# Kernel tuning notes

Measured on AMD Instinct MI355X. Metric: run time of the kernel, lower is better.

Reference implementation:

```python
import jax, jax.numpy as jnp
import numpy as np

N = 200_000   # total nodes across batch
D = 256       # input_dim (feature size)
B = 1024      # batch_size (number of graphs)
N_ITERS = 6


def setup_inputs() -> dict:
    key = jax.random.key(0)
    k0, k1, k2, k3, k4, k5 = jax.random.split(key, 6)
    s = 1.0 / np.sqrt(D)  # pytorch LSTM init: U(-1/sqrt(hidden), 1/sqrt(hidden))
    feat = jax.random.normal(k0, (N, D), dtype=jnp.float32)
    segment_ids = jnp.sort(jax.random.randint(k1, (N,), 0, B, dtype=jnp.int32))
    W_ih = jax.random.uniform(k2, (4 * D, 2 * D), minval=-s, maxval=s, dtype=jnp.float32)
    W_hh = jax.random.uniform(k3, (4 * D, D), minval=-s, maxval=s, dtype=jnp.float32)
    b_ih = jax.random.uniform(k4, (4 * D,), minval=-s, maxval=s, dtype=jnp.float32)
    b_hh = jax.random.uniform(k5, (4 * D,), minval=-s, maxval=s, dtype=jnp.float32)
    return {"feat": feat, "W_ih": W_ih, "W_hh": W_hh, "b_ih": b_ih,
            "b_hh": b_hh, "segment_ids": segment_ids, "batch_size": B}


def reference(feat, W_ih, W_hh, b_ih, b_hh, segment_ids, batch_size):
    H = W_hh.shape[1]
    dt = feat.dtype
    h = jnp.zeros((batch_size, H), dtype=dt)
    c = jnp.zeros((batch_size, H), dtype=dt)
    q_star = jnp.zeros((batch_size, 2 * H), dtype=dt)
    for _ in range(N_ITERS):
        # single-layer LSTM step on a length-1 sequence (pytorch gate order i,f,g,o)
        gates = q_star @ W_ih.T + h @ W_hh.T + b_ih + b_hh  # [B, 4H]
        gi, gf, gg, go = jnp.split(gates, 4, axis=-1)
        c = jax.nn.sigmoid(gf) * c + jax.nn.sigmoid(gi) * jnp.tanh(gg)
        h = jax.nn.sigmoid(go) * jnp.tanh(c)
        q = h  # [B, H]
        # e_i = <x_i, q_{graph(i)}>  (broadcast_nodes + dot)
        e = jnp.sum(feat * q[segment_ids], axis=-1)  # [N]
        # segment-wise stable softmax (softmax_nodes)
        emax = jax.ops.segment_max(e, segment_ids, num_segments=batch_size)
        ex = jnp.exp(e - emax[segment_ids])
        denom = jax.ops.segment_sum(ex, segment_ids, num_segments=batch_size)
        alpha = ex / denom[segment_ids]  # [N]
        # weighted sum readout (sum_nodes)
        readout = jax.ops.segment_sum(feat * alpha[:, None], segment_ids,
                                      num_segments=batch_size)  # [B, H]
        q_star = jnp.concatenate([q, readout], axis=-1)  # [B, 2H]
    return q_star
```

## Files before the change

kernel.cpp:

```cpp
#include <hip/hip_runtime.h>
#include <hip/hip_bf16.h>
#include <hip/hip_fp16.h>
#include <stdint.h>

#define D    256
#define K2   512
#define G4   1024

typedef __attribute__((ext_vector_type(8))) short  short8;
typedef __attribute__((ext_vector_type(4))) float  float4v;

__device__ inline short f2bf(float v) {
    __hip_bfloat16 b = __float2bfloat16(v);
    union { __hip_bfloat16 b; unsigned short u; } cv; cv.b = b;
    return (short)cv.u;
}
__device__ inline float bfs2f(short s) {
    union { unsigned int i; float f; } v;
    v.i = ((unsigned int)(unsigned short)s) << 16;
    return v.f;
}

__device__ inline float wave_sum64(float x) {
    union { float f; int i; } c, t;
#define DPP_ADD(CTRL, RM)                                                     \
    c.f = x;                                                                  \
    t.i = __builtin_amdgcn_update_dpp(0, c.i, (CTRL), (RM), 0xf, true);       \
    x += t.f;
    DPP_ADD(0x111, 0xf)
    DPP_ADD(0x112, 0xf)
    DPP_ADD(0x114, 0xf)
    DPP_ADD(0x118, 0xf)
    DPP_ADD(0x142, 0xa)
    DPP_ADD(0x143, 0xc)
#undef DPP_ADD
    union { float f; int i; } r; r.f = x;
    r.i = __builtin_amdgcn_readlane(r.i, 63);
    return r.f;
}

__global__ void k_bounds(const int* __restrict__ seg, int N, int B,
                         int* __restrict__ start) {
    int g = blockIdx.x * blockDim.x + threadIdx.x;
    if (g > B) return;
    int lo = 0, hi = N;
    while (lo < hi) { int mid = (lo + hi) >> 1; if (seg[mid] < g) lo = mid + 1; else hi = mid; }
    start[g] = lo;
}

__global__ void k_cvt(const float* __restrict__ feat, __half* __restrict__ feat16,
                      int total) {
    int i = (blockIdx.x * blockDim.x + threadIdx.x) * 8;
    int stride = gridDim.x * blockDim.x * 8;
    for (; i < total; i += stride) {
        float4v a = *(const float4v*)(feat + i);
        float4v b = *(const float4v*)(feat + i + 4);
        union { __half2 h2[4]; uint4 u; } o;
        o.h2[0] = __floats2half2_rn(a.x, a.y);
        o.h2[1] = __floats2half2_rn(a.z, a.w);
        o.h2[2] = __floats2half2_rn(b.x, b.y);
        o.h2[3] = __floats2half2_rn(b.z, b.w);
        *(uint4*)(feat16 + i) = o.u;
    }
}

__global__ void k_prep(const float* __restrict__ Wih,
                       const float* __restrict__ Whh,
                       const float* __restrict__ bih,
                       const float* __restrict__ bhh,
                       short* __restrict__ Wch, short* __restrict__ Wcl,
                       float* __restrict__ bsum) {
    int idx = blockIdx.x * blockDim.x + threadIdx.x;
    if (idx >= G4 * K2) return;
    int r = idx >> 9, cc = idx & (K2 - 1);
    float v = Wih[idx];
    if (cc < D) v += Whh[r * D + cc];
    short hi = f2bf(v);
    Wch[idx] = hi;
    Wcl[idx] = f2bf(v - bfs2f(hi));
    if (idx < G4) bsum[idx] = bih[idx] + bhh[idx];
}

__global__ __launch_bounds__(256) void k_gemm_lstm(
        const short* __restrict__ Xh, const short* __restrict__ Xl,
        const short* __restrict__ Wch, const short* __restrict__ Wcl,
        const float* __restrict__ bsum,
        float* __restrict__ c, float* __restrict__ h) {
    int wave = threadIdx.x >> 6, lane = threadIdx.x & 63;
    int row = lane & 15, quad = lane >> 4;
    int m0 = blockIdx.x * 16;
    int jbase = blockIdx.y * 64 + wave * 16;
    const short* pah = Xh  + (size_t)(m0 + row) * K2 + quad * 8;
    const short* pal = Xl  + (size_t)(m0 + row) * K2 + quad * 8;
    const short* pbh = Wch + (size_t)(jbase + row) * K2 + quad * 8;
    const short* pbl = Wcl + (size_t)(jbase + row) * K2 + quad * 8;
    float4v acc0 = {0,0,0,0}, acc1 = {0,0,0,0}, acc2 = {0,0,0,0}, acc3 = {0,0,0,0};
#pragma unroll
    for (int k = 0; k < K2; k += 32) {
        short8 ahi = *(const short8*)(pah + k);
        short8 alo = *(const short8*)(pal + k);
#define GATE_MFMA(ACC, OFF)                                                        \
        {                                                                          \
            short8 bh = *(const short8*)(pbh + (size_t)(OFF) * K2 + k);            \
            short8 bl = *(const short8*)(pbl + (size_t)(OFF) * K2 + k);            \
            ACC = __builtin_amdgcn_mfma_f32_16x16x32_bf16(ahi, bh, ACC, 0, 0, 0);  \
            ACC = __builtin_amdgcn_mfma_f32_16x16x32_bf16(alo, bh, ACC, 0, 0, 0);  \
            ACC = __builtin_amdgcn_mfma_f32_16x16x32_bf16(ahi, bl, ACC, 0, 0, 0);  \
        }
        GATE_MFMA(acc0, 0)
        GATE_MFMA(acc1, 256)
        GATE_MFMA(acc2, 512)
        GATE_MFMA(acc3, 768)
#undef GATE_MFMA
    }
    int j = jbase + (lane & 15);
    float bi = bsum[j], bf_ = bsum[j + 256], bg = bsum[j + 512], bo = bsum[j + 768];
#pragma unroll
    for (int i = 0; i < 4; i++) {
        int m = m0 + quad * 4 + i;
        size_t ix = (size_t)m * D + j;
        float gi = acc0[i] + bi, gf = acc1[i] + bf_, gg = acc2[i] + bg, go = acc3[i] + bo;
        float si = 1.f / (1.f + __expf(-gi));
        float sf = 1.f / (1.f + __expf(-gf));
        float so = 1.f / (1.f + __expf(-go));
        float cn = sf * c[ix] + si * tanhf(gg);
        float hn = so * tanhf(cn);
        c[ix] = cn;
        h[ix] = hn;
    }
}

__global__ __launch_bounds__(256) void k_attn(const __half* __restrict__ feat16,
                                              const int* __restrict__ start,
                                              const float* __restrict__ h,
                                              float* __restrict__ X,
                                              short* __restrict__ Xh,
                                              short* __restrict__ Xl, int N) {
    __shared__ float accs[4 * D];
    __shared__ float ms[4], ls[4];
    int g = blockIdx.x;
    int t = threadIdx.x;
    int lane = t & 63, wave = t >> 6;
    float hv = h[(size_t)g * D + t];
    {
        size_t ox = (size_t)g * K2 + t;
        X[ox] = hv;
        short hi = f2bf(hv);
        Xh[ox] = hi;
        Xl[ox] = f2bf(hv - bfs2f(hi));
    }
    int s = start[g], e = start[g + 1];
    s = max(0, min(s, N)); e = max(s, min(e, N));
    int cnt = e - s;
    if (cnt <= 0) {
        size_t ox = (size_t)g * K2 + D + t;
        X[ox] = 0.f; Xh[ox] = 0; Xl[ox] = 0;
        return;
    }
    const float NEG = -3.0e38f;
    float4v q = *(const float4v*)(h + (size_t)g * D + lane * 4);
    float m = NEG, l = 0.f;
    float4v acc = {0.f, 0.f, 0.f, 0.f};

    for (int n0 = wave * 4; n0 < cnt; n0 += 16) {
        uint2 raw[4];
#pragma unroll
        for (int r = 0; r < 4; r++) {
            int idx = n0 + r;
            int ci = (idx < cnt) ? (s + idx) : s;
            raw[r] = *((const uint2*)(feat16 + (size_t)ci * D) + lane);
        }
        float4v rows[4];
        float ev[4];
#pragma unroll
        for (int r = 0; r < 4; r++) {
            union { uint2 u; __half2 h2[2]; } cv; cv.u = raw[r];
            float2 f01 = __half22float2(cv.h2[0]);
            float2 f23 = __half22float2(cv.h2[1]);
            rows[r].x = f01.x; rows[r].y = f01.y; rows[r].z = f23.x; rows[r].w = f23.y;
            ev[r] = rows[r].x * q.x + rows[r].y * q.y + rows[r].z * q.z + rows[r].w * q.w;
        }
#pragma unroll
        for (int r = 0; r < 4; r++) ev[r] = wave_sum64(ev[r]);
        float mnew = m;
#pragma unroll
        for (int r = 0; r < 4; r++) {
            if (n0 + r >= cnt) ev[r] = NEG;
            mnew = fmaxf(mnew, ev[r]);
        }
        float alpha = __expf(m - mnew);
        float w[4];
        float wsum = 0.f;
#pragma unroll
        for (int r = 0; r < 4; r++) {
            w[r] = (n0 + r < cnt) ? __expf(ev[r] - mnew) : 0.f;
            wsum += w[r];
        }
        l = l * alpha + wsum;
        acc.x *= alpha; acc.y *= alpha; acc.z *= alpha; acc.w *= alpha;
#pragma unroll
        for (int r = 0; r < 4; r++) {
            acc.x += w[r] * rows[r].x;
            acc.y += w[r] * rows[r].y;
            acc.z += w[r] * rows[r].z;
            acc.w += w[r] * rows[r].w;
        }
        m = mnew;
    }

    *((float4v*)(accs + wave * D + lane * 4)) = acc;
    if (lane == 0) { ms[wave] = m; ls[wave] = l; }
    __syncthreads();
    float mt = fmaxf(fmaxf(ms[0], ms[1]), fmaxf(ms[2], ms[3]));
    float s0 = __expf(ms[0] - mt), s1 = __expf(ms[1] - mt);
    float s2 = __expf(ms[2] - mt), s3 = __expf(ms[3] - mt);
    float lt = ls[0] * s0 + ls[1] * s1 + ls[2] * s2 + ls[3] * s3;
    float val = (accs[t] * s0 + accs[D + t] * s1
               + accs[2 * D + t] * s2 + accs[3 * D + t] * s3) / lt;
    size_t ox = (size_t)g * K2 + D + t;
    X[ox] = val;
    short hi = f2bf(val);
    Xh[ox] = hi;
    Xl[ox] = f2bf(val - bfs2f(hi));
}

extern "C" void kernel_launch(void* const* d_in, const int* in_sizes, int n_in,
                              void* d_out, int out_size, void* d_ws, size_t ws_size,
                              hipStream_t stream) {
    const float* feat = (const float*)d_in[0];
    const float* Wih  = (const float*)d_in[1];
    const float* Whh  = (const float*)d_in[2];
    const float* bih  = (const float*)d_in[3];
    const float* bhh  = (const float*)d_in[4];
    const int*   seg  = (const int*)d_in[5];
    const int N = in_sizes[5];
    const int B = out_size / K2;
    const int total = N * D;

    char* ws = (char*)d_ws;
    size_t szC = (size_t)B * D * sizeof(float);
    float* c   = (float*)ws;
    float* h   = (float*)(ws + szC);
    short* Xh  = (short*)(ws + 2 * szC);
    short* Xl  = (short*)(ws + 2 * szC + (size_t)B * K2 * sizeof(short));
    short* Wch = (short*)(ws + 2 * szC + 2 * (size_t)B * K2 * sizeof(short));
    short* Wcl = (short*)((char*)Wch + (size_t)G4 * K2 * sizeof(short));
    float* bsum = (float*)((char*)Wcl + (size_t)G4 * K2 * sizeof(short));
    int*   start = (int*)((char*)bsum + (size_t)G4 * sizeof(float));
    __half* feat16 = (__half*)(ws + (size_t)16 * 1024 * 1024);

    float* X = (float*)d_out;

    hipMemsetAsync(ws, 0, 2 * szC + 2 * (size_t)B * K2 * sizeof(short), stream);
    k_cvt<<<8192, 256, 0, stream>>>(feat, feat16, total);
    k_prep<<<(G4 * K2 + 255) / 256, 256, 0, stream>>>(Wih, Whh, bih, bhh, Wch, Wcl, bsum);
    k_bounds<<<(B + 1 + 255) / 256, 256, 0, stream>>>(seg, N, B, start);

    for (int it = 0; it < 6; it++) {
        k_gemm_lstm<<<dim3(B / 16, 4), 256, 0, stream>>>(Xh, Xl, Wch, Wcl, bsum, c, h);
        k_attn<<<B, 256, 0, stream>>>(feat16, start, h, X, Xh, Xl, N);
    }
}
```

Baseline: 566.7 us.

## Fuse fp16 feature conversion into first attention pass; split LSTM GEMM across more blocks

```diff
diff --git a/kernel.cpp b/kernel.cpp
--- a/kernel.cpp
+++ b/kernel.cpp
@@ -48,22 +48,6 @@
     start[g] = lo;
 }
 
-__global__ void k_cvt(const float* __restrict__ feat, __half* __restrict__ feat16,
-                      int total) {
-    int i = (blockIdx.x * blockDim.x + threadIdx.x) * 8;
-    int stride = gridDim.x * blockDim.x * 8;
-    for (; i < total; i += stride) {
-        float4v a = *(const float4v*)(feat + i);
-        float4v b = *(const float4v*)(feat + i + 4);
-        union { __half2 h2[4]; uint4 u; } o;
-        o.h2[0] = __floats2half2_rn(a.x, a.y);
-        o.h2[1] = __floats2half2_rn(a.z, a.w);
-        o.h2[2] = __floats2half2_rn(b.x, b.y);
-        o.h2[3] = __floats2half2_rn(b.z, b.w);
-        *(uint4*)(feat16 + i) = o.u;
-    }
-}
-
 __global__ void k_prep(const float* __restrict__ Wih,
                        const float* __restrict__ Whh,
                        const float* __restrict__ bih,
@@ -81,7 +65,7 @@
     if (idx < G4) bsum[idx] = bih[idx] + bhh[idx];
 }
 
-__global__ __launch_bounds__(256) void k_gemm_lstm(
+__global__ __launch_bounds__(256, 4) void k_gemm_lstm(
         const short* __restrict__ Xh, const short* __restrict__ Xl,
         const short* __restrict__ Wch, const short* __restrict__ Wcl,
         const float* __restrict__ bsum,
@@ -89,53 +73,52 @@
     int wave = threadIdx.x >> 6, lane = threadIdx.x & 63;
     int row = lane & 15, quad = lane >> 4;
     int m0 = blockIdx.x * 16;
-    int jbase = blockIdx.y * 64 + wave * 16;
+    int jb = blockIdx.y * 16;
+    int wrow = wave * 256 + jb + row;
     const short* pah = Xh  + (size_t)(m0 + row) * K2 + quad * 8;
     const short* pal = Xl  + (size_t)(m0 + row) * K2 + quad * 8;
-    const short* pbh = Wch + (size_t)(jbase + row) * K2 + quad * 8;
-    const short* pbl = Wcl + (size_t)(jbase + row) * K2 + quad * 8;
-    float4v acc0 = {0,0,0,0}, acc1 = {0,0,0,0}, acc2 = {0,0,0,0}, acc3 = {0,0,0,0};
+    const short* pbh = Wch + (size_t)wrow * K2 + quad * 8;
+    const short* pbl = Wcl + (size_t)wrow * K2 + quad * 8;
+    float4v acc = {0, 0, 0, 0};
 #pragma unroll
     for (int k = 0; k < K2; k += 32) {
         short8 ahi = *(const short8*)(pah + k);
         short8 alo = *(const short8*)(pal + k);
-#define GATE_MFMA(ACC, OFF)                                                        \
-        {                                                                          \
-            short8 bh = *(const short8*)(pbh + (size_t)(OFF) * K2 + k);            \
-            short8 bl = *(const short8*)(pbl + (size_t)(OFF) * K2 + k);            \
-            ACC = __builtin_amdgcn_mfma_f32_16x16x32_bf16(ahi, bh, ACC, 0, 0, 0);  \
-            ACC = __builtin_amdgcn_mfma_f32_16x16x32_bf16(alo, bh, ACC, 0, 0, 0);  \
-            ACC = __builtin_amdgcn_mfma_f32_16x16x32_bf16(ahi, bl, ACC, 0, 0, 0);  \
-        }
-        GATE_MFMA(acc0, 0)
-        GATE_MFMA(acc1, 256)
-        GATE_MFMA(acc2, 512)
-        GATE_MFMA(acc3, 768)
-#undef GATE_MFMA
-    }
-    int j = jbase + (lane & 15);
-    float bi = bsum[j], bf_ = bsum[j + 256], bg = bsum[j + 512], bo = bsum[j + 768];
-#pragma unroll
-    for (int i = 0; i < 4; i++) {
-        int m = m0 + quad * 4 + i;
-        size_t ix = (size_t)m * D + j;
-        float gi = acc0[i] + bi, gf = acc1[i] + bf_, gg = acc2[i] + bg, go = acc3[i] + bo;
-        float si = 1.f / (1.f + __expf(-gi));
-        float sf = 1.f / (1.f + __expf(-gf));
-        float so = 1.f / (1.f + __expf(-go));
-        float cn = sf * c[ix] + si * tanhf(gg);
-        float hn = so * tanhf(cn);
-        c[ix] = cn;
-        h[ix] = hn;
-    }
-}
-
-__global__ __launch_bounds__(256) void k_attn(const __half* __restrict__ feat16,
-                                              const int* __restrict__ start,
-                                              const float* __restrict__ h,
-                                              float* __restrict__ X,
-                                              short* __restrict__ Xh,
-                                              short* __restrict__ Xl, int N) {
+        short8 bh  = *(const short8*)(pbh + k);
+        short8 bl  = *(const short8*)(pbl + k);
+        acc = __builtin_amdgcn_mfma_f32_16x16x32_bf16(ahi, bh, acc, 0, 0, 0);
+        acc = __builtin_amdgcn_mfma_f32_16x16x32_bf16(alo, bh, acc, 0, 0, 0);
+        acc = __builtin_amdgcn_mfma_f32_16x16x32_bf16(ahi, bl, acc, 0, 0, 0);
+    }
+    __shared__ float gl[4][16][17];
+#pragma unroll
+    for (int i = 0; i < 4; i++) gl[wave][quad * 4 + i][row] = acc[i];
+    __syncthreads();
+    int t = threadIdx.x;
+    int mi = t >> 4, jj = t & 15;
+    int j = jb + jj;
+    float gi = gl[0][mi][jj] + bsum[j];
+    float gf = gl[1][mi][jj] + bsum[j + 256];
+    float gg = gl[2][mi][jj] + bsum[j + 512];
+    float go = gl[3][mi][jj] + bsum[j + 768];
+    size_t ix = (size_t)(m0 + mi) * D + j;
+    float si = 1.f / (1.f + __expf(-gi));
+    float sf = 1.f / (1.f + __expf(-gf));
+    float so = 1.f / (1.f + __expf(-go));
+    float cn = sf * c[ix] + si * tanhf(gg);
+    float hn = so * tanhf(cn);
+    c[ix] = cn;
+    h[ix] = hn;
+}
+
+template <bool FIRST>
+__global__ __launch_bounds__(256) void k_attn_t(const float* __restrict__ feat32,
+                                                __half* __restrict__ feat16,
+                                                const int* __restrict__ start,
+                                                const float* __restrict__ h,
+                                                float* __restrict__ X,
+                                                short* __restrict__ Xh,
+                                                short* __restrict__ Xl, int N) {
     __shared__ float accs[4 * D];
     __shared__ float ms[4], ls[4];
     int g = blockIdx.x;
@@ -163,23 +146,44 @@
     float4v acc = {0.f, 0.f, 0.f, 0.f};
 
     for (int n0 = wave * 4; n0 < cnt; n0 += 16) {
-        uint2 raw[4];
-#pragma unroll
-        for (int r = 0; r < 4; r++) {
-            int idx = n0 + r;
-            int ci = (idx < cnt) ? (s + idx) : s;
-            raw[r] = *((const uint2*)(feat16 + (size_t)ci * D) + lane);
-        }
         float4v rows[4];
+        if (FIRST) {
+#pragma unroll
+            for (int r = 0; r < 4; r++) {
+                int idx = n0 + r;
+                int ci = (idx < cnt) ? (s + idx) : s;
+                rows[r] = *((const float4v*)(feat32 + (size_t)ci * D) + lane);
+            }
+#pragma unroll
+            for (int r = 0; r < 4; r++) {
+                int idx = n0 + r;
+                if (idx < cnt) {
+                    union { uint2 u; __half2 h2[2]; } cv;
+                    cv.h2[0] = __floats2half2_rn(rows[r].x, rows[r].y);
+                    cv.h2[1] = __floats2half2_rn(rows[r].z, rows[r].w);
+                    *((uint2*)(feat16 + (size_t)(s + idx) * D) + lane) = cv.u;
+                }
+            }
+        } else {
+            uint2 raw[4];
+#pragma unroll
+            for (int r = 0; r < 4; r++) {
+                int idx = n0 + r;
+                int ci = (idx < cnt) ? (s + idx) : s;
+                raw[r] = *((const uint2*)(feat16 + (size_t)ci * D) + lane);
+            }
+#pragma unroll
+            for (int r = 0; r < 4; r++) {
+                union { uint2 u; __half2 h2[2]; } cv; cv.u = raw[r];
+                float2 f01 = __half22float2(cv.h2[0]);
+                float2 f23 = __half22float2(cv.h2[1]);
+                rows[r].x = f01.x; rows[r].y = f01.y; rows[r].z = f23.x; rows[r].w = f23.y;
+            }
+        }
         float ev[4];
 #pragma unroll
-        for (int r = 0; r < 4; r++) {
-            union { uint2 u; __half2 h2[2]; } cv; cv.u = raw[r];
-            float2 f01 = __half22float2(cv.h2[0]);
-            float2 f23 = __half22float2(cv.h2[1]);
-            rows[r].x = f01.x; rows[r].y = f01.y; rows[r].z = f23.x; rows[r].w = f23.y;
+        for (int r = 0; r < 4; r++)
             ev[r] = rows[r].x * q.x + rows[r].y * q.y + rows[r].z * q.z + rows[r].w * q.w;
-        }
 #pragma unroll
         for (int r = 0; r < 4; r++) ev[r] = wave_sum64(ev[r]);
         float mnew = m;
@@ -235,7 +239,6 @@
     const int*   seg  = (const int*)d_in[5];
     const int N = in_sizes[5];
     const int B = out_size / K2;
-    const int total = N * D;
 
     char* ws = (char*)d_ws;
     size_t szC = (size_t)B * D * sizeof(float);
@@ -252,12 +255,14 @@
     float* X = (float*)d_out;
 
     hipMemsetAsync(ws, 0, 2 * szC + 2 * (size_t)B * K2 * sizeof(short), stream);
-    k_cvt<<<8192, 256, 0, stream>>>(feat, feat16, total);
     k_prep<<<(G4 * K2 + 255) / 256, 256, 0, stream>>>(Wih, Whh, bih, bhh, Wch, Wcl, bsum);
     k_bounds<<<(B + 1 + 255) / 256, 256, 0, stream>>>(seg, N, B, start);
 
     for (int it = 0; it < 6; it++) {
-        k_gemm_lstm<<<dim3(B / 16, 4), 256, 0, stream>>>(Xh, Xl, Wch, Wcl, bsum, c, h);
-        k_attn<<<B, 256, 0, stream>>>(feat16, start, h, X, Xh, Xl, N);
-    }
-}
+        k_gemm_lstm<<<dim3(B / 16, 16), 256, 0, stream>>>(Xh, Xl, Wch, Wcl, bsum, c, h);
+        if (it == 0)
+            k_attn_t<true ><<<B, 256, 0, stream>>>(feat, feat16, start, h, X, Xh, Xl, N);
+        else
+            k_attn_t<false><<<B, 256, 0, stream>>>(feat, feat16, start, h, X, Xh, Xl, N);
+    }
+}
```

New measurement: 605.7 us. 1.07x slower.

## Fuse all prep and iteration kernels into one cooperative persistent kernel

Applied to the files above, without the earlier changes.

```diff
diff --git a/kernel.cpp b/kernel.cpp
--- a/kernel.cpp
+++ b/kernel.cpp
@@ -1,11 +1,18 @@
 #include <hip/hip_runtime.h>
+#include <hip/hip_cooperative_groups.h>
 #include <hip/hip_bf16.h>
 #include <hip/hip_fp16.h>
 #include <stdint.h>
 
+namespace cg = cooperative_groups;
+
 #define D    256
 #define K2   512
 #define G4   1024
+#define B_   1024
+#define NBLK 512
+#define NTHR 256
+#define GSTRIDE (NBLK * NTHR)
 
 typedef __attribute__((ext_vector_type(8))) short  short8;
 typedef __attribute__((ext_vector_type(4))) float  float4v;
@@ -37,6 +44,191 @@
     union { float f; int i; } r; r.f = x;
     r.i = __builtin_amdgcn_readlane(r.i, 63);
     return r.f;
+}
+
+__global__ __launch_bounds__(NTHR, 2) void k_fused(
+        const float* __restrict__ feat32, __half* __restrict__ feat16,
+        const float* __restrict__ Wih,  const float* __restrict__ Whh,
+        const float* __restrict__ bih,  const float* __restrict__ bhh,
+        const int* __restrict__ seg, int N,
+        short* __restrict__ Wch, short* __restrict__ Wcl,
+        float* __restrict__ bsum, int* __restrict__ start,
+        short* __restrict__ Xh, short* __restrict__ Xl,
+        float* __restrict__ c,  float* __restrict__ h,
+        float* __restrict__ X) {
+    cg::grid_group grid = cg::this_grid();
+    const int b    = blockIdx.x;
+    const int t    = threadIdx.x;
+    const int gid  = b * NTHR + t;
+    const int lane = t & 63, wave = t >> 6;
+
+    __shared__ float gl[4][16][17];
+    __shared__ float accs[4 * D];
+    __shared__ float ms[4], ls[4];
+
+    c[gid] = 0.f; c[gid + GSTRIDE] = 0.f;
+    h[gid] = 0.f; h[gid + GSTRIDE] = 0.f;
+#pragma unroll
+    for (int i = 0; i < 4; i++) { Xh[gid + i * GSTRIDE] = 0; Xl[gid + i * GSTRIDE] = 0; }
+    for (int idx = gid; idx < G4 * K2; idx += GSTRIDE) {
+        int r = idx >> 9, cc = idx & (K2 - 1);
+        float v = Wih[idx];
+        if (cc < D) v += Whh[r * D + cc];
+        short hi = f2bf(v);
+        Wch[idx] = hi;
+        Wcl[idx] = f2bf(v - bfs2f(hi));
+        if (idx < G4) bsum[idx] = bih[idx] + bhh[idx];
+    }
+    if (gid <= B_) {
+        int lo = 0, hi = N;
+        while (lo < hi) { int mid = (lo + hi) >> 1; if (seg[mid] < gid) lo = mid + 1; else hi = mid; }
+        start[gid] = lo;
+    }
+    {
+        const int total = N * D;
+        for (int i = gid * 8; i < total; i += GSTRIDE * 8) {
+            float4v a = *(const float4v*)(feat32 + i);
+            float4v bb = *(const float4v*)(feat32 + i + 4);
+            union { __half2 h2[4]; uint4 u; } o;
+            o.h2[0] = __floats2half2_rn(a.x, a.y);
+            o.h2[1] = __floats2half2_rn(a.z, a.w);
+            o.h2[2] = __floats2half2_rn(bb.x, bb.y);
+            o.h2[3] = __floats2half2_rn(bb.z, bb.w);
+            *(uint4*)(feat16 + i) = o.u;
+        }
+    }
+    grid.sync();
+
+    for (int it = 0; it < 6; ++it) {
+        for (int vb = b; vb < 1024; vb += NBLK) {
+            int row = lane & 15, quad = lane >> 4;
+            int m0 = (vb & 63) * 16;
+            int jb = (vb >> 6) * 16;
+            int wrow = wave * 256 + jb + row;
+            const short* pah = Xh  + (size_t)(m0 + row) * K2 + quad * 8;
+            const short* pal = Xl  + (size_t)(m0 + row) * K2 + quad * 8;
+            const short* pbh = Wch + (size_t)wrow * K2 + quad * 8;
+            const short* pbl = Wcl + (size_t)wrow * K2 + quad * 8;
+            float4v acc = {0, 0, 0, 0};
+#pragma unroll
+            for (int k = 0; k < K2; k += 32) {
+                short8 ahi = *(const short8*)(pah + k);
+                short8 alo = *(const short8*)(pal + k);
+                short8 bh  = *(const short8*)(pbh + k);
+                short8 bl  = *(const short8*)(pbl + k);
+                acc = __builtin_amdgcn_mfma_f32_16x16x32_bf16(ahi, bh, acc, 0, 0, 0);
+                acc = __builtin_amdgcn_mfma_f32_16x16x32_bf16(alo, bh, acc, 0, 0, 0);
+                acc = __builtin_amdgcn_mfma_f32_16x16x32_bf16(ahi, bl, acc, 0, 0, 0);
+            }
+#pragma unroll
+            for (int i = 0; i < 4; i++) gl[wave][quad * 4 + i][row] = acc[i];
+            __syncthreads();
+            int mi = t >> 4, jj = t & 15;
+            int j = jb + jj;
+            float gi = gl[0][mi][jj] + bsum[j];
+            float gf = gl[1][mi][jj] + bsum[j + 256];
+            float gg = gl[2][mi][jj] + bsum[j + 512];
+            float go = gl[3][mi][jj] + bsum[j + 768];
+            size_t ix = (size_t)(m0 + mi) * D + j;
+            float si = 1.f / (1.f + __expf(-gi));
+            float sf = 1.f / (1.f + __expf(-gf));
+            float so = 1.f / (1.f + __expf(-go));
+            float cn = sf * c[ix] + si * tanhf(gg);
+            float hn = so * tanhf(cn);
+            c[ix] = cn;
+            h[ix] = hn;
+            __syncthreads();
+        }
+        grid.sync();
+
+        for (int g = b; g < B_; g += NBLK) {
+            float hv = h[(size_t)g * D + t];
+            {
+                size_t ox = (size_t)g * K2 + t;
+                X[ox] = hv;
+                short hi = f2bf(hv);
+                Xh[ox] = hi;
+                Xl[ox] = f2bf(hv - bfs2f(hi));
+            }
+            int s = start[g], e = start[g + 1];
+            s = max(0, min(s, N)); e = max(s, min(e, N));
+            int cnt = e - s;
+            if (cnt <= 0) {
+                size_t ox = (size_t)g * K2 + D + t;
+                X[ox] = 0.f; Xh[ox] = 0; Xl[ox] = 0;
+            } else {
+                const float NEG = -3.0e38f;
+                float4v q = *(const float4v*)(h + (size_t)g * D + lane * 4);
+                float m = NEG, l = 0.f;
+                float4v acc = {0.f, 0.f, 0.f, 0.f};
+
+                for (int n0 = wave * 4; n0 < cnt; n0 += 16) {
+                    uint2 raw[4];
+#pragma unroll
+                    for (int r = 0; r < 4; r++) {
+                        int idx = n0 + r;
+                        int ci = (idx < cnt) ? (s + idx) : s;
+                        raw[r] = *((const uint2*)(feat16 + (size_t)ci * D) + lane);
+                    }
+                    float4v rows[4];
+                    float ev[4];
+#pragma unroll
+                    for (int r = 0; r < 4; r++) {
+                        union { uint2 u; __half2 h2[2]; } cv; cv.u = raw[r];
+                        float2 f01 = __half22float2(cv.h2[0]);
+                        float2 f23 = __half22float2(cv.h2[1]);
+                        rows[r].x = f01.x; rows[r].y = f01.y;
+                        rows[r].z = f23.x; rows[r].w = f23.y;
+                        ev[r] = rows[r].x * q.x + rows[r].y * q.y
+                              + rows[r].z * q.z + rows[r].w * q.w;
+                    }
+#pragma unroll
+                    for (int r = 0; r < 4; r++) ev[r] = wave_sum64(ev[r]);
+                    float mnew = m;
+#pragma unroll
+                    for (int r = 0; r < 4; r++) {
+                        if (n0 + r >= cnt) ev[r] = NEG;
+                        mnew = fmaxf(mnew, ev[r]);
+                    }
+                    float alpha = __expf(m - mnew);
+                    float w[4];
+                    float wsum = 0.f;
+#pragma unroll
+                    for (int r = 0; r < 4; r++) {
+                        w[r] = (n0 + r < cnt) ? __expf(ev[r] - mnew) : 0.f;
+                        wsum += w[r];
+                    }
+                    l = l * alpha + wsum;
+                    acc.x *= alpha; acc.y *= alpha; acc.z *= alpha; acc.w *= alpha;
+#pragma unroll
+                    for (int r = 0; r < 4; r++) {
+                        acc.x += w[r] * rows[r].x;
+                        acc.y += w[r] * rows[r].y;
+                        acc.z += w[r] * rows[r].z;
+                        acc.w += w[r] * rows[r].w;
+                    }
+                    m = mnew;
+                }
+
+                *((float4v*)(accs + wave * D + lane * 4)) = acc;
+                if (lane == 0) { ms[wave] = m; ls[wave] = l; }
+                __syncthreads();
+                float mt = fmaxf(fmaxf(ms[0], ms[1]), fmaxf(ms[2], ms[3]));
+                float s0 = __expf(ms[0] - mt), s1 = __expf(ms[1] - mt);
+                float s2 = __expf(ms[2] - mt), s3 = __expf(ms[3] - mt);
+                float lt = ls[0] * s0 + ls[1] * s1 + ls[2] * s2 + ls[3] * s3;
+                float val = (accs[t] * s0 + accs[D + t] * s1
+                           + accs[2 * D + t] * s2 + accs[3 * D + t] * s3) / lt;
+                size_t ox = (size_t)g * K2 + D + t;
+                X[ox] = val;
+                short hi = f2bf(val);
+                Xh[ox] = hi;
+                Xl[ox] = f2bf(val - bfs2f(hi));
+            }
+            __syncthreads();
+        }
+        grid.sync();
+    }
 }
 
 __global__ void k_bounds(const int* __restrict__ seg, int N, int B,
@@ -233,9 +425,8 @@
     const float* bih  = (const float*)d_in[3];
     const float* bhh  = (const float*)d_in[4];
     const int*   seg  = (const int*)d_in[5];
-    const int N = in_sizes[5];
-    const int B = out_size / K2;
-    const int total = N * D;
+    int N = in_sizes[5];
+    const int B = B_;
 
     char* ws = (char*)d_ws;
     size_t szC = (size_t)B * D * sizeof(float);
@@ -251,13 +442,24 @@
 
     float* X = (float*)d_out;
 
-    hipMemsetAsync(ws, 0, 2 * szC + 2 * (size_t)B * K2 * sizeof(short), stream);
-    k_cvt<<<8192, 256, 0, stream>>>(feat, feat16, total);
-    k_prep<<<(G4 * K2 + 255) / 256, 256, 0, stream>>>(Wih, Whh, bih, bhh, Wch, Wcl, bsum);
-    k_bounds<<<(B + 1 + 255) / 256, 256, 0, stream>>>(seg, N, B, start);
-
-    for (int it = 0; it < 6; it++) {
-        k_gemm_lstm<<<dim3(B / 16, 4), 256, 0, stream>>>(Xh, Xl, Wch, Wcl, bsum, c, h);
-        k_attn<<<B, 256, 0, stream>>>(feat16, start, h, X, Xh, Xl, N);
-    }
-}
+    void* args[] = {
+        (void*)&feat, (void*)&feat16, (void*)&Wih, (void*)&Whh,
+        (void*)&bih,  (void*)&bhh,    (void*)&seg, (void*)&N,
+        (void*)&Wch,  (void*)&Wcl,    (void*)&bsum, (void*)&start,
+        (void*)&Xh,   (void*)&Xl,     (void*)&c,    (void*)&h, (void*)&X
+    };
+    hipError_t err = hipLaunchCooperativeKernel((const void*)k_fused,
+                                                dim3(NBLK), dim3(NTHR),
+                                                args, 0, stream);
+    if (err != hipSuccess) {
+        const int total = N * D;
+        hipMemsetAsync(ws, 0, 2 * szC + 2 * (size_t)B * K2 * sizeof(short), stream);
+        k_cvt<<<8192, 256, 0, stream>>>(feat, feat16, total);
+        k_prep<<<(G4 * K2 + 255) / 256, 256, 0, stream>>>(Wih, Whh, bih, bhh, Wch, Wcl, bsum);
+        k_bounds<<<(B + 1 + 255) / 256, 256, 0, stream>>>(seg, N, B, start);
+        for (int it = 0; it < 6; it++) {
+            k_gemm_lstm<<<dim3(B / 16, 4), 256, 0, stream>>>(Xh, Xl, Wch, Wcl, bsum, c, h);
+            k_attn<<<B, 256, 0, stream>>>(feat16, start, h, X, Xh, Xl, N);
+        }
+    }
+}
```

After: 1.383 ms. 2.44x slower.

## Fuse feature fp16 conversion into first attention pass and merge setup kernels

Applied to the files above, without the earlier changes.

```diff
diff --git a/kernel.cpp b/kernel.cpp
--- a/kernel.cpp
+++ b/kernel.cpp
@@ -6,6 +6,7 @@
 #define D    256
 #define K2   512
 #define G4   1024
+#define B_   1024
 
 typedef __attribute__((ext_vector_type(8))) short  short8;
 typedef __attribute__((ext_vector_type(4))) float  float4v;
@@ -39,39 +40,22 @@
     return r.f;
 }
 
-__global__ void k_bounds(const int* __restrict__ seg, int N, int B,
-                         int* __restrict__ start) {
-    int g = blockIdx.x * blockDim.x + threadIdx.x;
-    if (g > B) return;
-    int lo = 0, hi = N;
-    while (lo < hi) { int mid = (lo + hi) >> 1; if (seg[mid] < g) lo = mid + 1; else hi = mid; }
-    start[g] = lo;
-}
-
-__global__ void k_cvt(const float* __restrict__ feat, __half* __restrict__ feat16,
-                      int total) {
-    int i = (blockIdx.x * blockDim.x + threadIdx.x) * 8;
-    int stride = gridDim.x * blockDim.x * 8;
-    for (; i < total; i += stride) {
-        float4v a = *(const float4v*)(feat + i);
-        float4v b = *(const float4v*)(feat + i + 4);
-        union { __half2 h2[4]; uint4 u; } o;
-        o.h2[0] = __floats2half2_rn(a.x, a.y);
-        o.h2[1] = __floats2half2_rn(a.z, a.w);
-        o.h2[2] = __floats2half2_rn(b.x, b.y);
-        o.h2[3] = __floats2half2_rn(b.z, b.w);
-        *(uint4*)(feat16 + i) = o.u;
-    }
-}
-
-__global__ void k_prep(const float* __restrict__ Wih,
-                       const float* __restrict__ Whh,
-                       const float* __restrict__ bih,
-                       const float* __restrict__ bhh,
-                       short* __restrict__ Wch, short* __restrict__ Wcl,
-                       float* __restrict__ bsum) {
+__global__ __launch_bounds__(256) void k_prep2(
+        const float* __restrict__ Wih, const float* __restrict__ Whh,
+        const float* __restrict__ bih, const float* __restrict__ bhh,
+        const int* __restrict__ seg, int N,
+        short* __restrict__ Wch, short* __restrict__ Wcl,
+        float* __restrict__ bsum, int* __restrict__ start,
+        float* __restrict__ c, float* __restrict__ h,
+        short* __restrict__ Xh, short* __restrict__ Xl) {
     int idx = blockIdx.x * blockDim.x + threadIdx.x;
-    if (idx >= G4 * K2) return;
+    if (idx < B_ * D) { c[idx] = 0.f; h[idx] = 0.f; }
+    Xh[idx] = 0; Xl[idx] = 0;
+    if (idx <= B_) {
+        int lo = 0, hi = N;
+        while (lo < hi) { int mid = (lo + hi) >> 1; if (seg[mid] < idx) lo = mid + 1; else hi = mid; }
+        start[idx] = lo;
+    }
     int r = idx >> 9, cc = idx & (K2 - 1);
     float v = Wih[idx];
     if (cc < D) v += Whh[r * D + cc];
@@ -130,12 +114,14 @@
     }
 }
 
-__global__ __launch_bounds__(256) void k_attn(const __half* __restrict__ feat16,
-                                              const int* __restrict__ start,
-                                              const float* __restrict__ h,
-                                              float* __restrict__ X,
-                                              short* __restrict__ Xh,
-                                              short* __restrict__ Xl, int N) {
+template <bool FIRST>
+__global__ __launch_bounds__(256) void k_attn_t(const float* __restrict__ feat32,
+                                                __half* __restrict__ feat16,
+                                                const int* __restrict__ start,
+                                                const float* __restrict__ h,
+                                                float* __restrict__ X,
+                                                short* __restrict__ Xh,
+                                                short* __restrict__ Xl, int N) {
     __shared__ float accs[4 * D];
     __shared__ float ms[4], ls[4];
     int g = blockIdx.x;
@@ -162,50 +148,86 @@
     float m = NEG, l = 0.f;
     float4v acc = {0.f, 0.f, 0.f, 0.f};
 
-    for (int n0 = wave * 4; n0 < cnt; n0 += 16) {
-        uint2 raw[4];
+    float4v rows[4];
+    uint2   raw[4];
+    int n0 = wave * 4;
+    if (n0 < cnt) {
 #pragma unroll
         for (int r = 0; r < 4; r++) {
             int idx = n0 + r;
             int ci = (idx < cnt) ? (s + idx) : s;
-            raw[r] = *((const uint2*)(feat16 + (size_t)ci * D) + lane);
+            if (FIRST) rows[r] = *((const float4v*)(feat32 + (size_t)ci * D) + lane);
+            else       raw[r]  = *((const uint2*)(feat16 + (size_t)ci * D) + lane);
         }
-        float4v rows[4];
-        float ev[4];
-#pragma unroll
-        for (int r = 0; r < 4; r++) {
-            union { uint2 u; __half2 h2[2]; } cv; cv.u = raw[r];
-            float2 f01 = __half22float2(cv.h2[0]);
-            float2 f23 = __half22float2(cv.h2[1]);
-            rows[r].x = f01.x; rows[r].y = f01.y; rows[r].z = f23.x; rows[r].w = f23.y;
-            ev[r] = rows[r].x * q.x + rows[r].y * q.y + rows[r].z * q.z + rows[r].w * q.w;
+        for (; n0 < cnt; n0 += 16) {
+            float4v rowsn[4];
+            uint2   rawn[4];
+            int n1 = n0 + 16;
+#pragma unroll
+            for (int r = 0; r < 4; r++) {
+                int idx = n1 + r;
+                int ci = (idx < cnt) ? (s + idx) : s;
+                if (FIRST) rowsn[r] = *((const float4v*)(feat32 + (size_t)ci * D) + lane);
+                else       rawn[r]  = *((const uint2*)(feat16 + (size_t)ci * D) + lane);
+            }
+            if (FIRST) {
+#pragma unroll
+                for (int r = 0; r < 4; r++) {
+                    int idx = n0 + r;
+                    if (idx < cnt) {
+                        union { uint2 u; __half2 h2[2]; } cv;
+                        cv.h2[0] = __floats2half2_rn(rows[r].x, rows[r].y);
+                        cv.h2[1] = __floats2half2_rn(rows[r].z, rows[r].w);
+                        *((uint2*)(feat16 + (size_t)(s + idx) * D) + lane) = cv.u;
+                    }
+                }
+            } else {
+#pragma unroll
+                for (int r = 0; r < 4; r++) {
+                    union { uint2 u; __half2 h2[2]; } cv; cv.u = raw[r];
+                    float2 f01 = __half22float2(cv.h2[0]);
+                    float2 f23 = __half22float2(cv.h2[1]);
+                    rows[r].x = f01.x; rows[r].y = f01.y;
+                    rows[r].z = f23.x; rows[r].w = f23.y;
+                }
+            }
+            float ev[4];
+#pragma unroll
+            for (int r = 0; r < 4; r++)
+                ev[r] = rows[r].x * q.x + rows[r].y * q.y
+                      + rows[r].z * q.z + rows[r].w * q.w;
+#pragma unroll
+            for (int r = 0; r < 4; r++) ev[r] = wave_sum64(ev[r]);
+            float mnew = m;
+#pragma unroll
+            for (int r = 0; r < 4; r++) {
+                if (n0 + r >= cnt) ev[r] = NEG;
+                mnew = fmaxf(mnew, ev[r]);
+            }
+            float alpha = __expf(m - mnew);
+            float w[4];
+            float wsum = 0.f;
+#pragma unroll
+            for (int r = 0; r < 4; r++) {
+                w[r] = (n0 + r < cnt) ? __expf(ev[r] - mnew) : 0.f;
+                wsum += w[r];
+            }
+            l = l * alpha + wsum;
+            acc.x *= alpha; acc.y *= alpha; acc.z *= alpha; acc.w *= alpha;
+#pragma unroll
+            for (int r = 0; r < 4; r++) {
+                acc.x += w[r] * rows[r].x;
+                acc.y += w[r] * rows[r].y;
+                acc.z += w[r] * rows[r].z;
+                acc.w += w[r] * rows[r].w;
+            }
+            m = mnew;
+#pragma unroll
+            for (int r = 0; r < 4; r++) {
+                if (FIRST) rows[r] = rowsn[r];
+                else       raw[r]  = rawn[r];
+            }
         }
-#pragma unroll
-        for (int r = 0; r < 4; r++) ev[r] = wave_sum64(ev[r]);
-        float mnew = m;
-#pragma unroll
-        for (int r = 0; r < 4; r++) {
-            if (n0 + r >= cnt) ev[r] = NEG;
-            mnew = fmaxf(mnew, ev[r]);
-        }
-        float alpha = __expf(m - mnew);
-        float w[4];
-        float wsum = 0.f;
-#pragma unroll
-        for (int r = 0; r < 4; r++) {
-            w[r] = (n0 + r < cnt) ? __expf(ev[r] - mnew) : 0.f;
-            wsum += w[r];
-        }
-        l = l * alpha + wsum;
-        acc.x *= alpha; acc.y *= alpha; acc.z *= alpha; acc.w *= alpha;
-#pragma unroll
-        for (int r = 0; r < 4; r++) {
-            acc.x += w[r] * rows[r].x;
-            acc.y += w[r] * rows[r].y;
-            acc.z += w[r] * rows[r].z;
-            acc.w += w[r] * rows[r].w;
-        }
-        m = mnew;
     }
 
     *((float4v*)(accs + wave * D + lane * 4)) = acc;
@@ -234,8 +256,7 @@
     const float* bhh  = (const float*)d_in[4];
     const int*   seg  = (const int*)d_in[5];
     const int N = in_sizes[5];
-    const int B = out_size / K2;
-    const int total = N * D;
+    const int B = B_;
 
     char* ws = (char*)d_ws;
     size_t szC = (size_t)B * D * sizeof(float);
@@ -251,13 +272,14 @@
 
     float* X = (float*)d_out;
 
-    hipMemsetAsync(ws, 0, 2 * szC + 2 * (size_t)B * K2 * sizeof(short), stream);
-    k_cvt<<<8192, 256, 0, stream>>>(feat, feat16, total);
-    k_prep<<<(G4 * K2 + 255) / 256, 256, 0, stream>>>(Wih, Whh, bih, bhh, Wch, Wcl, bsum);
-    k_bounds<<<(B + 1 + 255) / 256, 256, 0, stream>>>(seg, N, B, start);
+    k_prep2<<<G4 * K2 / 256, 256, 0, stream>>>(Wih, Whh, bih, bhh, seg, N,
+                                               Wch, Wcl, bsum, start, c, h, Xh, Xl);
 
     for (int it = 0; it < 6; it++) {
         k_gemm_lstm<<<dim3(B / 16, 4), 256, 0, stream>>>(Xh, Xl, Wch, Wcl, bsum, c, h);
-        k_attn<<<B, 256, 0, stream>>>(feat16, start, h, X, Xh, Xl, N);
-    }
-}
+        if (it == 0)
+            k_attn_t<true ><<<B, 256, 0, stream>>>(feat, feat16, start, h, X, Xh, Xl, N);
+        else
+            k_attn_t<false><<<B, 256, 0, stream>>>(feat, feat16, start, h, X, Xh, Xl, N);
+    }
+}
```

After: 546.0 us. 3.6% less time.
